# Performance work log

Hardware: AMD Instinct MI355X
Metric: run time of the kernel (lower is better)

## Reference

```python
import jax, jax.numpy as jnp
import numpy as np

B, S, E = 8, 2048, 1024


def setup_inputs() -> dict:
    key = jax.random.key(0)
    ks = jax.random.split(key, 8)
    scale = 1.0 / np.sqrt(E)
    x = jax.random.normal(ks[0], (B, S, E), dtype=jnp.float32)
    Wq = jax.random.uniform(ks[1], (E, E), jnp.float32, -scale, scale)
    bq = jax.random.uniform(ks[2], (E,), jnp.float32, -scale, scale)
    Wk = jax.random.uniform(ks[3], (E, E), jnp.float32, -scale, scale)
    bk = jax.random.uniform(ks[4], (E,), jnp.float32, -scale, scale)
    Wv = jax.random.uniform(ks[5], (E, E), jnp.float32, -scale, scale)
    bv = jax.random.uniform(ks[6], (E,), jnp.float32, -scale, scale)
    # key-padding mask: True = fill position (broadcasts over query dim)
    mask = jax.random.randint(ks[7], (B, 1, S), 0, 2) > 0
    return {"x": x, "Wq": Wq, "bq": bq, "Wk": Wk, "bk": bk, "Wv": Wv, "bv": bv, "mask": mask}


def reference(x, Wq, bq, Wk, bk, Wv, bv, mask):
    # torch Linear: y = x @ W.T + b
    q = jnp.einsum('bse,fe->bsf', x, Wq) + bq
    k = jnp.einsum('bse,fe->bsf', x, Wk) + bk
    v = jnp.einsum('bse,fe->bsf', x, Wv) + bv
    inv_sqrt_d = 1.0 / jnp.sqrt(jnp.asarray(E, x.dtype))
    A = jnp.einsum('bqe,bke->bqk', q, k) * inv_sqrt_d  # (B, S, S)
    # non-standard masked_fill: fills with 1e-9 (NOT -inf), pre-softmax
    A = jnp.where(mask, jnp.asarray(1e-9, A.dtype), A)
    A = jax.nn.softmax(A, axis=-1)
    out = jnp.einsum('bqk,bke->bqe', A, v)
    # dropout is identity at inference
    return out
```

## Files before the change

kernel.cpp:

```cpp
#include <hip/hip_runtime.h>
#include <hip/hip_bf16.h>

#define B_ 8
#define S_ 2048
#define E_ 1024

using f32x4 = __attribute__((ext_vector_type(4))) float;
using s16x8 = __attribute__((ext_vector_type(8))) short;
using u16x8 = __attribute__((ext_vector_type(8))) unsigned short;

typedef __attribute__((address_space(1))) unsigned int glb_u32;
typedef __attribute__((address_space(3))) unsigned int lds_u32;

#define FENCE() __builtin_amdgcn_sched_barrier(0)

static __device__ __forceinline__ unsigned short f2bf(float f) {
    union { float f; unsigned int u; } v; v.f = f;
    unsigned int u = v.u;
    u += 0x7FFFu + ((u >> 16) & 1u);
    return (unsigned short)(u >> 16);
}
static __device__ __forceinline__ float bf2f(unsigned short h) {
    union { unsigned int u; float f; } v; v.u = ((unsigned int)h) << 16;
    return v.f;
}

__global__ __launch_bounds__(256) void mask_canon_kernel(
    const unsigned char* __restrict__ src, unsigned char* __restrict__ dst, int n)
{
    __shared__ int flags;
    if (threadIdx.x == 0) flags = 0;
    __syncthreads();
    int f = 0;
    for (int j = threadIdx.x; j < n; j += 256) {
        unsigned char b = src[j];
        if (b) {
            int p = j & 3;
            if (p == 1) f |= 1;
            if (p >= 2) f |= 2;
        }
    }
    if (f) atomicOr(&flags, f);
    __syncthreads();
    const int fl = flags;
    for (int i = threadIdx.x; i < n; i += 256) {
        unsigned char v;
        if (fl & 1)      v = (unsigned char)(src[i] != 0);
        else if (fl & 2) v = (unsigned char)(((const float*)(const void*)src)[i] != 0.0f);
        else             v = (unsigned char)(((const int*)(const void*)src)[i] != 0);
        dst[i] = v;
    }
}

__global__ __launch_bounds__(256) void cvt_all_kernel(
    const float* __restrict__ x,  unsigned short* __restrict__ xb,
    const float* __restrict__ w0, unsigned short* __restrict__ d0,
    const float* __restrict__ w1, unsigned short* __restrict__ d1,
    const float* __restrict__ w2, unsigned short* __restrict__ d2,
    int nx8, int nw8)
{
    const int total = nx8 + 3 * nw8;
    const int stride = gridDim.x * 256;
    for (int i = blockIdx.x * 256 + threadIdx.x; i < total; i += stride) {
        const float* s; unsigned short* d; int k;
        if (i < nx8)                { s = x;  d = xb; k = i; }
        else if (i < nx8 + nw8)     { s = w0; d = d0; k = i - nx8; }
        else if (i < nx8 + 2 * nw8) { s = w1; d = d1; k = i - nx8 - nw8; }
        else                        { s = w2; d = d2; k = i - nx8 - 2 * nw8; }
        float4 a = *(const float4*)(s + (size_t)k * 8);
        float4 b = *(const float4*)(s + (size_t)k * 8 + 4);
        u16x8 o;
        o[0]=f2bf(a.x); o[1]=f2bf(a.y); o[2]=f2bf(a.z); o[3]=f2bf(a.w);
        o[4]=f2bf(b.x); o[5]=f2bf(b.y); o[6]=f2bf(b.z); o[7]=f2bf(b.w);
        *(u16x8*)(d + (size_t)k * 8) = o;
    }
}

__global__ __launch_bounds__(256) void invrs_kernel(
    const float* __restrict__ psum, float* __restrict__ invrs, int n)
{
    int i = blockIdx.x * 256 + threadIdx.x;
    if (i < n) {
        const float* p = psum + (size_t)i * 8;
        float s = ((p[0] + p[1]) + (p[2] + p[3])) + ((p[4] + p[5]) + (p[6] + p[7]));
        invrs[i] = 1.0f / s;
    }
}

template<int EPI>
__global__ __launch_bounds__(512, 2) void gemm256(
    const unsigned short* __restrict__ A, const unsigned short* __restrict__ B,
    void* __restrict__ Cout,
    long long sAz, long long sBz, long long sCz,
    int lda, int ldb, int ldc, int K,
    const unsigned char* __restrict__ mask, int maskStride, float scale,
    const float* __restrict__ bias,
    const unsigned short* __restrict__ B2, const float* __restrict__ bias2,
    void* __restrict__ Cout2, float* __restrict__ aux)
{
    __shared__ unsigned short lds[65536];
    const int tid = threadIdx.x;
    const int lane = tid & 63, w = tid >> 6;
    const int wr = w >> 2, wc = w & 3;
    const int fr = lane & 15, ch = lane >> 4;

    const int gx = gridDim.x, gy = gridDim.y;
    const int nwg = gx * gy * gridDim.z;
    int bid = blockIdx.x + gx * (blockIdx.y + gy * blockIdx.z);
    bid = (bid & 7) * (nwg >> 3) + (bid >> 3);
    const int bx = bid % gx; int tmp = bid / gx;
    const int by = tmp % gy; const int bz = tmp / gy;

    const unsigned short* Ab = A + (size_t)bz * sAz;
    const unsigned short* Bb = B + (size_t)bz * sBz;
    const float* biasv = bias;
    void* Coutv = Cout;
    const int m0 = by * 256;
    int n0 = bx * 256;
    if constexpr (EPI == 4) {
        if (n0 >= 1024) { Bb = B2; biasv = bias2; Coutv = Cout2; n0 -= 1024; }
    }

    const int rdlane = fr * 32 + ((ch * 8) ^ ((fr & 8) ? 16 : 0));
    const int local = (lane * 16) ^ (lane & 32);
    const int rloc = local >> 6;
    const int cloc = (local >> 4) & 3;

    f32x4 acc[8][4] = {};
    const int NT = K >> 6;

    auto STAGE = [&](const unsigned short* __restrict__ src, int ld, int base,
                     int ts, int half, int matoff, unsigned bo) {
        const int k0 = ts * 64;
        const int rowb = half * 128 + w * 16;
        #pragma unroll
        for (int kk = 0; kk < 2; ++kk) {
            const unsigned short* g = src + (size_t)(base + rowb + rloc) * ld
                                          + (k0 + kk * 32 + cloc * 8);
            __builtin_amdgcn_global_load_lds((const glb_u32*)g,
                (lds_u32*)&lds[bo + matoff + kk * 8192 + rowb * 32], 16, 0, 0);
        }
    };

    STAGE(Ab, lda, m0, 0, 0, 0, 0);      STAGE(Ab, lda, m0, 0, 1, 0, 0);
    STAGE(Bb, ldb, n0, 0, 0, 16384, 0);  STAGE(Bb, ldb, n0, 0, 1, 16384, 0);
    STAGE(Ab, lda, m0, 1, 0, 0, 32768);  STAGE(Ab, lda, m0, 1, 1, 0, 32768);
    STAGE(Bb, ldb, n0, 1, 0, 16384, 32768);
    asm volatile("s_waitcnt vmcnt(6)" ::: "memory");
    __builtin_amdgcn_s_barrier();

    for (int t = 0; t < NT; ++t) {
        const unsigned bo = (unsigned)(t & 1) * 32768u;
        const unsigned nbo = bo ^ 32768u;
        const int tp1 = (t + 1 < NT) ? t + 1 : NT - 1;
        const int tp2 = (t + 2 < NT) ? t + 2 : NT - 1;

        s16x8 af[8][2], bfv[4][2];
        #pragma unroll
        for (int i = 0; i < 4; ++i)
            #pragma unroll
            for (int kk = 0; kk < 2; ++kk)
                af[i][kk] = *(const s16x8*)&lds[bo + kk * 8192 + (wr * 128 + i * 16) * 32 + rdlane];
        #pragma unroll
        for (int j = 0; j < 2; ++j)
            #pragma unroll
            for (int kk = 0; kk < 2; ++kk)
                bfv[j][kk] = *(const s16x8*)&lds[bo + 16384 + kk * 8192 + (wc * 64 + j * 16) * 32 + rdlane];
        FENCE();
        #pragma unroll
        for (int i = 4; i < 8; ++i)
            #pragma unroll
            for (int kk = 0; kk < 2; ++kk)
                af[i][kk] = *(const s16x8*)&lds[bo + kk * 8192 + (wr * 128 + i * 16) * 32 + rdlane];
        #pragma unroll
        for (int j = 2; j < 4; ++j)
            #pragma unroll
            for (int kk = 0; kk < 2; ++kk)
                bfv[j][kk] = *(const s16x8*)&lds[bo + 16384 + kk * 8192 + (wc * 64 + j * 16) * 32 + rdlane];
        STAGE(Bb, ldb, n0, tp1, 1, 16384, nbo);
        FENCE();
        asm volatile("s_waitcnt lgkmcnt(12)" ::: "memory");
        FENCE();
        __builtin_amdgcn_s_setprio(1);
        #pragma unroll
        for (int kk = 0; kk < 2; ++kk)
            #pragma unroll
            for (int i = 0; i < 4; ++i)
                #pragma unroll
                for (int j = 0; j < 2; ++j)
                    acc[i][j] = __builtin_amdgcn_mfma_f32_16x16x32_bf16(af[i][kk], bfv[j][kk], acc[i][j], 0, 0, 0);
        __builtin_amdgcn_s_setprio(0);
        FENCE();
        asm volatile("s_waitcnt lgkmcnt(0)" ::: "memory");
        FENCE();
        __builtin_amdgcn_s_setprio(1);
        #pragma unroll
        for (int kk = 0; kk < 2; ++kk)
            #pragma unroll
            for (int i = 0; i < 4; ++i)
                #pragma unroll
                for (int j = 0; j < 2; ++j)
                    acc[i][2 + j] = __builtin_amdgcn_mfma_f32_16x16x32_bf16(af[i][kk], bfv[2 + j][kk], acc[i][2 + j], 0, 0, 0);
        __builtin_amdgcn_s_setprio(0);
        FENCE();
        __builtin_amdgcn_s_barrier();
        FENCE();
        STAGE(Bb, ldb, n0, tp2, 0, 16384, bo);
        STAGE(Ab, lda, m0, tp2, 0, 0, bo);
        STAGE(Ab, lda, m0, tp2, 1, 0, bo);
        FENCE();
        __builtin_amdgcn_s_setprio(1);
        #pragma unroll
        for (int kk = 0; kk < 2; ++kk)
            #pragma unroll
            for (int i = 0; i < 4; ++i)
                #pragma unroll
                for (int j = 0; j < 2; ++j)
                    acc[4 + i][j] = __builtin_amdgcn_mfma_f32_16x16x32_bf16(af[4 + i][kk], bfv[j][kk], acc[4 + i][j], 0, 0, 0);
        #pragma unroll
        for (int kk = 0; kk < 2; ++kk)
            #pragma unroll
            for (int i = 0; i < 4; ++i)
                #pragma unroll
                for (int j = 0; j < 2; ++j)
                    acc[4 + i][2 + j] = __builtin_amdgcn_mfma_f32_16x16x32_bf16(af[4 + i][kk], bfv[2 + j][kk], acc[4 + i][2 + j], 0, 0, 0);
        __builtin_amdgcn_s_setprio(0);
        FENCE();
        asm volatile("s_waitcnt vmcnt(6)" ::: "memory");
        FENCE();
        __builtin_amdgcn_s_barrier();
    }

    asm volatile("s_waitcnt vmcnt(0) lgkmcnt(0)" ::: "memory");
    __builtin_amdgcn_s_barrier();

    if constexpr (EPI == 1) {
        float* Cb = (float*)Coutv + (size_t)bz * sCz;
        const float* invrs = aux;
        float* lf = (float*)lds;
        #pragma unroll
        for (int p = 0; p < 2; ++p) {
            if (p == 1) __syncthreads();
            #pragma unroll
            for (int j = 0; j < 4; ++j) {
                const int lcol = wc * 64 + j * 16 + fr;
                #pragma unroll
                for (int i = 0; i < 4; ++i)
                    #pragma unroll
                    for (int r = 0; r < 4; ++r) {
                        const int lrow = wr * 64 + i * 16 + ch * 4 + r;
                        lf[lrow * 256 + lcol] = acc[4 * p + i][j][r];
                    }
            }
            __syncthreads();
            #pragma unroll
            for (int s = 0; s < 16; ++s) {
                const int lrow = s * 8 + (tid >> 6);
                const int colf = (tid & 63) * 4;
                float4 v = *(const float4*)&lf[lrow * 256 + colf];
                const int mrow = m0 + ((lrow >= 64) ? 128 : 0) + p * 64 + (lrow & 63);
                const float irs = invrs[(size_t)bz * S_ + mrow];
                v.x *= irs; v.y *= irs; v.z *= irs; v.w *= irs;
                *(float4*)&Cb[(size_t)mrow * ldc + n0 + colf] = v;
            }
        }
    } else {
        unsigned short* Cb = (unsigned short*)Coutv + (size_t)bz * sCz;
        const unsigned char* mb = (EPI == 0) ? mask + (size_t)bz * maskStride : nullptr;
        #pragma unroll
        for (int j = 0; j < 4; ++j) {
            const int lcol = wc * 64 + j * 16 + fr;
            bool msk = false; float bn = 0.f;
            if constexpr (EPI == 0) msk = mb[n0 + lcol] != 0;
            if constexpr (EPI == 2 || EPI == 4) bn = biasv[n0 + lcol];
            #pragma unroll
            for (int i = 0; i < 8; ++i) {
                #pragma unroll
                for (int r = 0; r < 4; ++r) {
                    const int lrow = wr * 128 + i * 16 + ch * 4 + r;
                    float val;
                    if constexpr (EPI == 0)      val = msk ? 1.0f : __expf(acc[i][j][r] * scale);
                    else if constexpr (EPI == 2 || EPI == 4) val = acc[i][j][r] + bn;
                    else                         val = acc[i][j][r] + biasv[m0 + lrow];
                    lds[lrow * 256 + lcol] = f2bf(val);
                }
            }
        }
        __syncthreads();
        if constexpr (EPI == 0) {
            const int row = tid >> 1, half = tid & 1;
            float s = 0.f;
            #pragma unroll
            for (int c = 0; c < 16; ++c) {
                const int cc = (c + row) & 15;
                u16x8 v8 = *(const u16x8*)&lds[row * 256 + half * 128 + cc * 8];
                #pragma unroll
                for (int e = 0; e < 8; ++e) s += bf2f(v8[e]);
            }
            s += __shfl_xor(s, 1, 64);
            if (half == 0)
                aux[((size_t)bz * S_ + m0 + row) * 8 + bx] = s;
        }
        #pragma unroll
        for (int s = 0; s < 16; ++s) {
            const int lrow = s * 16 + (tid >> 5);
            const int colu = (tid & 31) * 8;
            u16x8 v = *(const u16x8*)&lds[lrow * 256 + colu];
            *(u16x8*)&Cb[(size_t)(m0 + lrow) * ldc + n0 + colu] = v;
        }
    }
}

extern "C" void kernel_launch(void* const* d_in, const int* in_sizes, int n_in,
                              void* d_out, int out_size, void* d_ws, size_t ws_size,
                              hipStream_t stream)
{
    const float* x  = (const float*)d_in[0];
    const float* Wq = (const float*)d_in[1];
    const float* bq = (const float*)d_in[2];
    const float* Wk = (const float*)d_in[3];
    const float* bk = (const float*)d_in[4];
    const float* Wv = (const float*)d_in[5];
    const float* bv = (const float*)d_in[6];
    const unsigned char* mraw = (const unsigned char*)d_in[7];

    const int BS = B_ * S_;
    unsigned short* Qb = (unsigned short*)d_ws;
    unsigned short* Kb = Qb + (size_t)BS * E_;
    unsigned short* VT = Kb + (size_t)BS * E_;
    unsigned short* Sc = VT + (size_t)BS * E_;
    unsigned short* xb = Sc;
    unsigned short* Wqb = Sc + (size_t)BS * E_;
    unsigned short* Wkb = Wqb + (size_t)E_ * E_;
    unsigned short* Wvb = Wkb + (size_t)E_ * E_;
    unsigned char* mcanon = (unsigned char*)(Sc + (size_t)B_ * S_ * S_);
    float* psum = (float*)(mcanon + 65536);
    float* invr = psum + (size_t)BS * 8;

    mask_canon_kernel<<<1, 256, 0, stream>>>(mraw, mcanon, BS);

    cvt_all_kernel<<<2048, 256, 0, stream>>>(
        x, xb, Wq, Wqb, Wk, Wkb, Wv, Wvb, BS * E_ / 8, E_ * E_ / 8);

    gemm256<4><<<dim3(2048 / 256, BS / 256), 512, 0, stream>>>(
        xb, Wqb, (void*)Qb, 0, 0, 0, E_, E_, E_, E_, nullptr, 0, 1.0f, bq,
        Wkb, bk, (void*)Kb, nullptr);
    gemm256<3><<<dim3(BS / 256, E_ / 256), 512, 0, stream>>>(
        Wvb, xb, (void*)VT, 0, 0, 0, E_, E_, BS, E_, nullptr, 0, 1.0f, bv,
        nullptr, nullptr, nullptr, nullptr);

    gemm256<0><<<dim3(S_ / 256, S_ / 256, B_), 512, 0, stream>>>(
        Qb, Kb, (void*)Sc,
        (long long)S_ * E_, (long long)S_ * E_, (long long)S_ * S_,
        E_, E_, S_, E_, mcanon, S_, 0.03125f, nullptr,
        nullptr, nullptr, nullptr, psum);

    invrs_kernel<<<BS / 256, 256, 0, stream>>>(psum, invr, BS);

    gemm256<1><<<dim3(E_ / 256, S_ / 256, B_), 512, 0, stream>>>(
        Sc, VT, d_out,
        (long long)S_ * S_, (long long)S_, (long long)S_ * E_,
        S_, BS, E_, S_, nullptr, 0, 1.0f, nullptr,
        nullptr, nullptr, nullptr, invr);
}
```

Measured before the change: 309.2 us.

## Switch GEMM mainloop to triple-buffered K=32 tiles with one barrier per step

The K-step shrinks from 64 to 32, and the two-buffer scheme with split staging becomes a three-buffer rotation. The full tile two steps ahead is prefetched with global_load_lds while the current tile is consumed, and each iteration has a single barrier. The goal is to keep prefetch distance while removing the mid-loop barrier and the partial-stage choreography. In exchange the loop runs twice as many iterations, each with half the MFMA work to hide load latency and barrier overhead.

```diff
diff --git a/kernel.cpp b/kernel.cpp
--- a/kernel.cpp
+++ b/kernel.cpp
@@ -127,108 +127,77 @@
     const int cloc = (local >> 4) & 3;
 
     f32x4 acc[8][4] = {};
-    const int NT = K >> 6;
+    const int NT = K >> 5;
 
     auto STAGE = [&](const unsigned short* __restrict__ src, int ld, int base,
-                     int ts, int half, int matoff, unsigned bo) {
-        const int k0 = ts * 64;
+                     int ts, int half, int matoff, unsigned bufo) {
         const int rowb = half * 128 + w * 16;
-        #pragma unroll
-        for (int kk = 0; kk < 2; ++kk) {
-            const unsigned short* g = src + (size_t)(base + rowb + rloc) * ld
-                                          + (k0 + kk * 32 + cloc * 8);
-            __builtin_amdgcn_global_load_lds((const glb_u32*)g,
-                (lds_u32*)&lds[bo + matoff + kk * 8192 + rowb * 32], 16, 0, 0);
-        }
+        const unsigned short* g = src + (size_t)(base + rowb + rloc) * ld
+                                      + (ts * 32 + cloc * 8);
+        __builtin_amdgcn_global_load_lds((const glb_u32*)g,
+            (lds_u32*)&lds[bufo + matoff + rowb * 32], 16, 0, 0);
     };
-
-    STAGE(Ab, lda, m0, 0, 0, 0, 0);      STAGE(Ab, lda, m0, 0, 1, 0, 0);
-    STAGE(Bb, ldb, n0, 0, 0, 16384, 0);  STAGE(Bb, ldb, n0, 0, 1, 16384, 0);
-    STAGE(Ab, lda, m0, 1, 0, 0, 32768);  STAGE(Ab, lda, m0, 1, 1, 0, 32768);
-    STAGE(Bb, ldb, n0, 1, 0, 16384, 32768);
-    asm volatile("s_waitcnt vmcnt(6)" ::: "memory");
+    auto STAGE_TILE = [&](int ts, unsigned bufo) {
+        STAGE(Ab, lda, m0, ts, 0, 0, bufo);
+        STAGE(Ab, lda, m0, ts, 1, 0, bufo);
+        STAGE(Bb, ldb, n0, ts, 0, 8192, bufo);
+        STAGE(Bb, ldb, n0, ts, 1, 8192, bufo);
+    };
+
+    STAGE_TILE(0, 0);
+    STAGE_TILE((1 < NT) ? 1 : 0, 16384);
+    asm volatile("s_waitcnt vmcnt(4)" ::: "memory");
     __builtin_amdgcn_s_barrier();
 
+    unsigned cur = 0, nxt = 16384, stg = 32768;
     for (int t = 0; t < NT; ++t) {
-        const unsigned bo = (unsigned)(t & 1) * 32768u;
-        const unsigned nbo = bo ^ 32768u;
-        const int tp1 = (t + 1 < NT) ? t + 1 : NT - 1;
         const int tp2 = (t + 2 < NT) ? t + 2 : NT - 1;
 
-        s16x8 af[8][2], bfv[4][2];
+        s16x8 af[8], bfv[4];
         #pragma unroll
         for (int i = 0; i < 4; ++i)
-            #pragma unroll
-            for (int kk = 0; kk < 2; ++kk)
-                af[i][kk] = *(const s16x8*)&lds[bo + kk * 8192 + (wr * 128 + i * 16) * 32 + rdlane];
+            af[i] = *(const s16x8*)&lds[cur + (wr * 128 + i * 16) * 32 + rdlane];
         #pragma unroll
         for (int j = 0; j < 2; ++j)
-            #pragma unroll
-            for (int kk = 0; kk < 2; ++kk)
-                bfv[j][kk] = *(const s16x8*)&lds[bo + 16384 + kk * 8192 + (wc * 64 + j * 16) * 32 + rdlane];
+            bfv[j] = *(const s16x8*)&lds[cur + 8192 + (wc * 64 + j * 16) * 32 + rdlane];
         FENCE();
         #pragma unroll
         for (int i = 4; i < 8; ++i)
-            #pragma unroll
-            for (int kk = 0; kk < 2; ++kk)
-                af[i][kk] = *(const s16x8*)&lds[bo + kk * 8192 + (wr * 128 + i * 16) * 32 + rdlane];
+            af[i] = *(const s16x8*)&lds[cur + (wr * 128 + i * 16) * 32 + rdlane];
         #pragma unroll
         for (int j = 2; j < 4; ++j)
-            #pragma unroll
-            for (int kk = 0; kk < 2; ++kk)
-                bfv[j][kk] = *(const s16x8*)&lds[bo + 16384 + kk * 8192 + (wc * 64 + j * 16) * 32 + rdlane];
-        STAGE(Bb, ldb, n0, tp1, 1, 16384, nbo);
-        FENCE();
-        asm volatile("s_waitcnt lgkmcnt(12)" ::: "memory");
+            bfv[j] = *(const s16x8*)&lds[cur + 8192 + (wc * 64 + j * 16) * 32 + rdlane];
+        STAGE_TILE(tp2, stg);
+        FENCE();
+        asm volatile("s_waitcnt lgkmcnt(6)" ::: "memory");
         FENCE();
         __builtin_amdgcn_s_setprio(1);
         #pragma unroll
-        for (int kk = 0; kk < 2; ++kk)
-            #pragma unroll
-            for (int i = 0; i < 4; ++i)
-                #pragma unroll
-                for (int j = 0; j < 2; ++j)
-                    acc[i][j] = __builtin_amdgcn_mfma_f32_16x16x32_bf16(af[i][kk], bfv[j][kk], acc[i][j], 0, 0, 0);
+        for (int i = 0; i < 4; ++i)
+            #pragma unroll
+            for (int j = 0; j < 2; ++j)
+                acc[i][j] = __builtin_amdgcn_mfma_f32_16x16x32_bf16(af[i], bfv[j], acc[i][j], 0, 0, 0);
         __builtin_amdgcn_s_setprio(0);
         FENCE();
         asm volatile("s_waitcnt lgkmcnt(0)" ::: "memory");
         FENCE();
         __builtin_amdgcn_s_setprio(1);
         #pragma unroll
-        for (int kk = 0; kk < 2; ++kk)
-            #pragma unroll
-            for (int i = 0; i < 4; ++i)
-                #pragma unroll
-                for (int j = 0; j < 2; ++j)
-                    acc[i][2 + j] = __builtin_amdgcn_mfma_f32_16x16x32_bf16(af[i][kk], bfv[2 + j][kk], acc[i][2 + j], 0, 0, 0);
+        for (int i = 0; i < 4; ++i)
+            #pragma unroll
+            for (int j = 2; j < 4; ++j)
+                acc[i][j] = __builtin_amdgcn_mfma_f32_16x16x32_bf16(af[i], bfv[j], acc[i][j], 0, 0, 0);
+        #pragma unroll
+        for (int i = 4; i < 8; ++i)
+            #pragma unroll
+            for (int j = 0; j < 4; ++j)
+                acc[i][j] = __builtin_amdgcn_mfma_f32_16x16x32_bf16(af[i], bfv[j], acc[i][j], 0, 0, 0);
         __builtin_amdgcn_s_setprio(0);
         FENCE();
+        asm volatile("s_waitcnt vmcnt(4)" ::: "memory");
+        FENCE();
         __builtin_amdgcn_s_barrier();
-        FENCE();
-        STAGE(Bb, ldb, n0, tp2, 0, 16384, bo);
-        STAGE(Ab, lda, m0, tp2, 0, 0, bo);
-        STAGE(Ab, lda, m0, tp2, 1, 0, bo);
-        FENCE();
-        __builtin_amdgcn_s_setprio(1);
-        #pragma unroll
-        for (int kk = 0; kk < 2; ++kk)
-            #pragma unroll
-            for (int i = 0; i < 4; ++i)
-                #pragma unroll
-                for (int j = 0; j < 2; ++j)
-                    acc[4 + i][j] = __builtin_amdgcn_mfma_f32_16x16x32_bf16(af[4 + i][kk], bfv[j][kk], acc[4 + i][j], 0, 0, 0);
-        #pragma unroll
-        for (int kk = 0; kk < 2; ++kk)
-            #pragma unroll
-            for (int i = 0; i < 4; ++i)
-                #pragma unroll
-                for (int j = 0; j < 2; ++j)
-                    acc[4 + i][2 + j] = __builtin_amdgcn_mfma_f32_16x16x32_bf16(af[4 + i][kk], bfv[2 + j][kk], acc[4 + i][2 + j], 0, 0, 0);
-        __builtin_amdgcn_s_setprio(0);
-        FENCE();
-        asm volatile("s_waitcnt vmcnt(6)" ::: "memory");
-        FENCE();
-        __builtin_amdgcn_s_barrier();
+        const unsigned tmpb = cur; cur = nxt; nxt = stg; stg = tmpb;
     }
 
     asm volatile("s_waitcnt vmcnt(0) lgkmcnt(0)" ::: "memory");
```

Measured after the change: 317.2 us. 2.6% more time.
